# Kernel optimization log

Hardware: AMD Instinct MI355X
Metric: run time of the kernel (lower is better)

Reference implementation:

```python
import jax, jax.numpy as jnp
import numpy as np
import math

GRID = 32          # config.grid_size
DIM = 256          # sparse_head_dim = n_embd * mlp_internal_dim_multiplier // n_head
B, H = 8, 8        # batch, n_head
N = GRID * GRID    # tokens = grid_size^2


def get_freqs_2d(h, w, dim, theta=10000.0):
    """2D RoPE angles; returns (cos, sin) each of shape (h*w, dim//2)."""
    dim_half = dim // 2
    inv = 1.0 / theta ** (np.arange(0, dim_half, 2).astype(np.float32) / dim_half)
    fx = np.outer(np.arange(w, dtype=np.float32), inv)   # (w, dim_half//2)
    fy = np.outer(np.arange(h, dtype=np.float32), inv)   # (h, dim_half//2)
    fx_grid = np.broadcast_to(fx[None, :, :], (h, w, fx.shape[1]))
    fy_grid = np.broadcast_to(fy[:, None, :], (h, w, fy.shape[1]))
    ang = np.concatenate([fx_grid, fy_grid], axis=-1).reshape(h * w, dim_half)
    return jnp.asarray(np.cos(ang)), jnp.asarray(np.sin(ang))


def apply_rotary(x, cos, sin):
    # x: (B,H,N,D) viewed as complex pairs along last dim; complex multiply by e^{i*ang}
    xr = x.reshape(*x.shape[:-1], -1, 2)
    x0, x1 = xr[..., 0], xr[..., 1]          # (B,H,N,D/2)
    out_re = x0 * cos - x1 * sin
    out_im = x0 * sin + x1 * cos
    return jnp.stack([out_re, out_im], axis=-1).reshape(x.shape)


def setup_inputs() -> dict:
    key = jax.random.key(0)
    k1, k2, k3 = jax.random.split(key, 3)
    shape = (B, H, N, DIM)
    return {
        "Q": jax.random.normal(k1, shape, dtype=jnp.float32),
        "K": jax.random.normal(k2, shape, dtype=jnp.float32),
        "V": jax.random.normal(k3, shape, dtype=jnp.float32),
    }


def reference(Q, K, V):
    cos, sin = get_freqs_2d(GRID, GRID, DIM)  # (N, DIM/2) each, broadcast over B,H
    QR = apply_rotary(Q, cos, sin)
    KR = apply_rotary(K, cos, sin)
    scores = jnp.einsum('bhnd,bhmd->bhnm', QR, KR) / math.sqrt(QR.shape[-1])
    attn = jax.nn.softmax(scores, axis=-1)
    return jnp.einsum('bhnm,bhmd->bhnd', attn, V)
```

## Files before the change

### kernel.cpp

```cpp
#include <hip/hip_runtime.h>
#include <hip/hip_bf16.h>
#include <cstdint>

#define BH     64
#define NTOK   1024
#define DDIM   256
#define QT     128
#define KTILE  32
#define NITER  (NTOK / KTILE)
#define PP     40

typedef __bf16 bf16x8 __attribute__((ext_vector_type(8)));
typedef float  f32x4  __attribute__((ext_vector_type(4)));
typedef float  f32x16 __attribute__((ext_vector_type(16)));

__device__ __forceinline__ unsigned short f2bf(float f) {
    __bf16 b = (__bf16)f;
    return __builtin_bit_cast(unsigned short, b);
}
__device__ __forceinline__ float bf2f(unsigned short u) {
    return __builtin_bit_cast(float, ((unsigned int)u) << 16);
}
__device__ __forceinline__ unsigned int pack2(float lo, float hi) {
    return (unsigned int)f2bf(lo) | ((unsigned int)f2bf(hi) << 16);
}

typedef const __attribute__((address_space(1))) unsigned int* gas_t;
typedef __attribute__((address_space(3))) unsigned int* las_t;
__device__ __forceinline__ void gload16(const void* g, void* l) {
    __builtin_amdgcn_global_load_lds((gas_t)g, (las_t)l, 16, 0, 0);
}

#define ANG_C    (13.287712379549449f / 64.0f)
#define SM_SCALE (1.4426950408889634f / 16.0f)

__global__ __launch_bounds__(256) void prep(const float* __restrict__ K,
                                            const float* __restrict__ V,
                                            unsigned short* __restrict__ KR,
                                            unsigned short* __restrict__ VT) {
    __shared__ unsigned short tile[64 * 264];
    int tid = threadIdx.x;
    if (blockIdx.x < 8192) {
        int gid = blockIdx.x * 256 + tid;
        int chunk = gid & 31;
        int t = (gid >> 5) & (NTOK - 1);
        float x = (float)(t & 31), y = (float)(t >> 5);
        const float4 a = *(const float4*)(K + (size_t)gid * 8);
        const float4 b = *(const float4*)(K + (size_t)gid * 8 + 4);
        float f[8] = {a.x, a.y, a.z, a.w, b.x, b.y, b.z, b.w};
        unsigned int o[4];
#pragma unroll
        for (int p = 0; p < 4; ++p) {
            int j = chunk * 4 + p;
            float pos = (j < 64) ? x : y;
            float inv = __builtin_exp2f(-(float)(j & 63) * ANG_C);
            float s, c;
            __sincosf(pos * inv, &s, &c);
            float x0 = f[2 * p], x1 = f[2 * p + 1];
            o[p] = pack2(x0 * c - x1 * s, x0 * s + x1 * c);
        }
        uint4 ov; ov.x = o[0]; ov.y = o[1]; ov.z = o[2]; ov.w = o[3];
        *(uint4*)(KR + (size_t)gid * 8) = ov;
        return;
    }
    int vb = blockIdx.x - 8192;
    int bh = vb >> 4;
    int tbase = (vb & 15) * 64;
    const float* src = V + ((size_t)bh * NTOK + tbase) * DDIM;
#pragma unroll
    for (int i = 0; i < 8; ++i) {
        int flat = i * 2048 + tid * 8;
        int tl = flat >> 8, col = flat & 255;
        const float4 a = *(const float4*)(src + (size_t)tl * DDIM + col);
        const float4 b = *(const float4*)(src + (size_t)tl * DDIM + col + 4);
        uint4 ov;
        ov.x = pack2(a.x, a.y); ov.y = pack2(a.z, a.w);
        ov.z = pack2(b.x, b.y); ov.w = pack2(b.z, b.w);
        *(uint4*)(tile + tl * 264 + col) = ov;
    }
    __syncthreads();
    unsigned short* dst = VT + (size_t)bh * ((size_t)DDIM * NTOK) + tbase;
#pragma unroll
    for (int i = 0; i < 8; ++i) {
        int task = i * 256 + tid;
        int d = task >> 3, tq = task & 7;
        unsigned int o[4];
#pragma unroll
        for (int k = 0; k < 4; ++k) {
            unsigned short lo = tile[(tq * 8 + 2 * k    ) * 264 + d];
            unsigned short hi = tile[(tq * 8 + 2 * k + 1) * 264 + d];
            o[k] = (unsigned int)lo | ((unsigned int)hi << 16);
        }
        uint4 ov; ov.x = o[0]; ov.y = o[1]; ov.z = o[2]; ov.w = o[3];
        *(uint4*)(dst + (size_t)d * NTOK + tq * 8) = ov;
    }
}

__global__ __launch_bounds__(256, 2) void flash_attn(
        const float* __restrict__ Q,
        const unsigned short* __restrict__ KR,
        const unsigned short* __restrict__ VTg,
        float* __restrict__ Out) {
    __shared__ unsigned short KT[2][KTILE * DDIM];
    __shared__ unsigned short VTl[2][DDIM * KTILE];
    __shared__ unsigned short PB[4][32 * PP];

    const int tid = threadIdx.x;
    const int wave = tid >> 6, lane = tid & 63;
    const int l31 = lane & 31, h = lane >> 5;
    const int b = blockIdx.x;
    const int bh = (b & 7) + ((b >> 6) << 3);
    const int qbase = ((b >> 3) & 7) * QT;

    const unsigned short* krB = KR + (size_t)bh * ((size_t)NTOK * DDIM);
    const unsigned short* vtB = VTg + (size_t)bh * ((size_t)DDIM * NTOK);

    bf16x8 qfrag[16];
    {
        const int qtok = qbase + wave * 32 + l31;
        const float x = (float)(qtok & 31), y = (float)(qtok >> 5);
        const float* qrow = Q + ((size_t)bh * NTOK + qtok) * DDIM;
#pragma unroll
        for (int cc = 0; cc < 16; ++cc) {
            const float4 a = *(const float4*)(qrow + cc * 16 + h * 8);
            const float4 b2 = *(const float4*)(qrow + cc * 16 + h * 8 + 4);
            float f[8] = {a.x, a.y, a.z, a.w, b2.x, b2.y, b2.z, b2.w};
            unsigned int po[4];
#pragma unroll
            for (int p = 0; p < 4; ++p) {
                int j = cc * 8 + h * 4 + p;
                float pos = (j < 64) ? x : y;
                float inv = __builtin_exp2f(-(float)(j & 63) * ANG_C);
                float s, c;
                __sincosf(pos * inv, &s, &c);
                float x0 = f[2 * p], x1 = f[2 * p + 1];
                po[p] = pack2(x0 * c - x1 * s, x0 * s + x1 * c);
            }
            uint4 pk; pk.x = po[0]; pk.y = po[1]; pk.z = po[2]; pk.w = po[3];
            qfrag[cc] = __builtin_bit_cast(bf16x8, pk);
        }
    }
    asm volatile("s_waitcnt vmcnt(0)" ::: "memory");

    f32x16 o[8] = {};
    float lsum[16] = {};

    int kOff[4], vOff[4];
#pragma unroll
    for (int j = 0; j < 4; ++j) {
        int f = wave * 256 + j * 64 + lane;
        int rf = f >> 5, sf = f & 31;
        kOff[j] = rf * 256 + ((sf ^ (rf & 7)) * 8);
        int d0 = ((f >> 2) ^ (f >> 4)) & 1;
        int dv = ((f >> 3) << 1) | d0;
        int cv = (f & 3) ^ (dv & 3);
        vOff[j] = dv * NTOK + cv * 8;
    }
    const int kx = l31 & 7;
    const int vrd0 = ((4 * l31 + 0 + h) ^ kx) * 8;
    const int vrd1 = ((4 * l31 + 2 + h) ^ kx) * 8;

#pragma unroll
    for (int j = 0; j < 4; ++j)
        gload16(krB + kOff[j], &KT[0][wave * 2048 + j * 512]);
#pragma unroll
    for (int j = 0; j < 4; ++j)
        gload16(vtB + vOff[j], &VTl[0][wave * 2048 + j * 512]);

    unsigned short* pbw = &PB[wave][0];

    for (int it = 0; it < NITER; ++it) {
        const int cur = it & 1;
        if (it + 1 < NITER) {
            const int kb = (it + 1) * KTILE;
            const unsigned short* krT = krB + (size_t)kb * DDIM;
            const unsigned short* vtT = vtB + kb;
            const int nxt = cur ^ 1;
#pragma unroll
            for (int j = 0; j < 4; ++j)
                gload16(krT + kOff[j], &KT[nxt][wave * 2048 + j * 512]);
#pragma unroll
            for (int j = 0; j < 4; ++j)
                gload16(vtT + vOff[j], &VTl[nxt][wave * 2048 + j * 512]);
            asm volatile("s_waitcnt vmcnt(8)" ::: "memory");
        } else {
            asm volatile("s_waitcnt vmcnt(0)" ::: "memory");
        }
        __builtin_amdgcn_s_barrier();

        f32x16 sc = {};
        const unsigned short* ktb = KT[cur];
        __builtin_amdgcn_s_setprio(1);
#pragma unroll
        for (int cc = 0; cc < 16; ++cc) {
            const int sl = ((2 * cc + h) ^ kx) * 8;
            bf16x8 kb_ = *(const bf16x8*)(ktb + l31 * 256 + sl);
            sc = __builtin_amdgcn_mfma_f32_32x32x16_bf16(qfrag[cc], kb_, sc, 0, 0, 0);
        }
        __builtin_amdgcn_s_setprio(0);

#pragma unroll
        for (int r = 0; r < 16; ++r) {
            float p = __builtin_exp2f(sc[r] * SM_SCALE);
            unsigned short pb = f2bf(p);
            pbw[((r & 3) + 8 * (r >> 2) + 4 * h) * PP + l31] = pb;
            lsum[r] += bf2f(pb);
        }
        bf16x8 pa0 = *(const bf16x8*)(pbw + l31 * PP + h * 8);
        bf16x8 pa1 = *(const bf16x8*)(pbw + l31 * PP + 16 + h * 8);

        const unsigned short* vtb = VTl[cur];
        __builtin_amdgcn_s_setprio(1);
#pragma unroll
        for (int nt = 0; nt < 8; ++nt) {
            bf16x8 v0 = *(const bf16x8*)(vtb + nt * 1024 + vrd0);
            bf16x8 v1 = *(const bf16x8*)(vtb + nt * 1024 + vrd1);
            o[nt] = __builtin_amdgcn_mfma_f32_32x32x16_bf16(pa0, v0, o[nt], 0, 0, 0);
            o[nt] = __builtin_amdgcn_mfma_f32_32x32x16_bf16(pa1, v1, o[nt], 0, 0, 0);
        }
        __builtin_amdgcn_s_setprio(0);

        asm volatile("s_waitcnt lgkmcnt(0)" ::: "memory");
        __builtin_amdgcn_s_barrier();
    }

#pragma unroll
    for (int r = 0; r < 16; ++r) {
        float s = lsum[r];
        s += __shfl_xor(s, 1);
        s += __shfl_xor(s, 2);
        s += __shfl_xor(s, 4);
        s += __shfl_xor(s, 8);
        s += __shfl_xor(s, 16);
        float rl = 1.0f / s;
        const int row = (r & 3) + 8 * (r >> 2) + 4 * h;
        float* orow =
            Out + ((size_t)bh * NTOK + qbase + wave * 32 + row) * DDIM;
#pragma unroll
        for (int nt = 0; nt < 8; ++nt)
            orow[nt * 32 + l31] = o[nt][r] * rl;
    }
}

extern "C" void kernel_launch(void* const* d_in, const int* in_sizes, int n_in,
                              void* d_out, int out_size, void* d_ws, size_t ws_size,
                              hipStream_t stream) {
    const float* Q = (const float*)d_in[0];
    const float* K = (const float*)d_in[1];
    const float* V = (const float*)d_in[2];
    unsigned short* KR = (unsigned short*)d_ws;
    unsigned short* VT = KR + (size_t)BH * NTOK * DDIM;
    float* O = (float*)d_out;

    prep<<<8192 + BH * (NTOK / 64), 256, 0, stream>>>(K, V, KR, VT);
    flash_attn<<<BH * (NTOK / QT), 256, 0, stream>>>(Q, KR, VT, O);
}
```

Before: 349.0 us.

## Compute transposed scores to keep P in registers, dropping the LDS round-trip

Swaps the MFMA operands so the score tile comes out transposed (keys by queries). Each lane can then build the P operand for the PV matmul from its own registers plus cross-half shuffles, with no write to and read from an LDS scratch buffer. Row sums become per-lane partial sums reduced once at the end. The V shared-memory swizzle is redesigned to match, and RoPE sin/cos now uses the hardware revolution-based sin/cos instructions. The shuffle packing adds cross-lane traffic, and the V swizzle change could introduce bank conflicts.

```diff
diff --git a/kernel.cpp b/kernel.cpp
--- a/kernel.cpp
+++ b/kernel.cpp
@@ -8,10 +8,8 @@
 #define QT     128
 #define KTILE  32
 #define NITER  (NTOK / KTILE)
-#define PP     40
 
 typedef __bf16 bf16x8 __attribute__((ext_vector_type(8)));
-typedef float  f32x4  __attribute__((ext_vector_type(4)));
 typedef float  f32x16 __attribute__((ext_vector_type(16)));
 
 __device__ __forceinline__ unsigned short f2bf(float f) {
@@ -23,6 +21,12 @@
 }
 __device__ __forceinline__ unsigned int pack2(float lo, float hi) {
     return (unsigned int)f2bf(lo) | ((unsigned int)f2bf(hi) << 16);
+}
+
+__device__ __forceinline__ void sincos_rev(float rev, float* s, float* c) {
+    float fr = rev - __builtin_floorf(rev);
+    *s = __builtin_amdgcn_sinf(fr);
+    *c = __builtin_amdgcn_cosf(fr);
 }
 
 typedef const __attribute__((address_space(1))) unsigned int* gas_t;
@@ -32,6 +36,7 @@
 }
 
 #define ANG_C    (13.287712379549449f / 64.0f)
+#define L2_2PI   2.6514961294723187f
 #define SM_SCALE (1.4426950408889634f / 16.0f)
 
 __global__ __launch_bounds__(256) void prep(const float* __restrict__ K,
@@ -53,9 +58,9 @@
         for (int p = 0; p < 4; ++p) {
             int j = chunk * 4 + p;
             float pos = (j < 64) ? x : y;
-            float inv = __builtin_exp2f(-(float)(j & 63) * ANG_C);
+            float invr = __builtin_exp2f(-(float)(j & 63) * ANG_C - L2_2PI);
             float s, c;
-            __sincosf(pos * inv, &s, &c);
+            sincos_rev(pos * invr, &s, &c);
             float x0 = f[2 * p], x1 = f[2 * p + 1];
             o[p] = pack2(x0 * c - x1 * s, x0 * s + x1 * c);
         }
@@ -103,7 +108,6 @@
         float* __restrict__ Out) {
     __shared__ unsigned short KT[2][KTILE * DDIM];
     __shared__ unsigned short VTl[2][DDIM * KTILE];
-    __shared__ unsigned short PB[4][32 * PP];
 
     const int tid = threadIdx.x;
     const int wave = tid >> 6, lane = tid & 63;
@@ -130,9 +134,9 @@
             for (int p = 0; p < 4; ++p) {
                 int j = cc * 8 + h * 4 + p;
                 float pos = (j < 64) ? x : y;
-                float inv = __builtin_exp2f(-(float)(j & 63) * ANG_C);
+                float invr = __builtin_exp2f(-(float)(j & 63) * ANG_C - L2_2PI);
                 float s, c;
-                __sincosf(pos * inv, &s, &c);
+                sincos_rev(pos * invr, &s, &c);
                 float x0 = f[2 * p], x1 = f[2 * p + 1];
                 po[p] = pack2(x0 * c - x1 * s, x0 * s + x1 * c);
             }
@@ -143,7 +147,7 @@
     asm volatile("s_waitcnt vmcnt(0)" ::: "memory");
 
     f32x16 o[8] = {};
-    float lsum[16] = {};
+    float lsum[4] = {};
 
     int kOff[4], vOff[4];
 #pragma unroll
@@ -151,14 +155,14 @@
         int f = wave * 256 + j * 64 + lane;
         int rf = f >> 5, sf = f & 31;
         kOff[j] = rf * 256 + ((sf ^ (rf & 7)) * 8);
-        int d0 = ((f >> 2) ^ (f >> 4)) & 1;
-        int dv = ((f >> 3) << 1) | d0;
-        int cv = (f & 3) ^ (dv & 3);
-        vOff[j] = dv * NTOK + cv * 8;
+        int gI = f ^ ((f >> 3) & 3);
+        vOff[j] = (gI >> 2) * NTOK + (gI & 3) * 8;
     }
     const int kx = l31 & 7;
-    const int vrd0 = ((4 * l31 + 0 + h) ^ kx) * 8;
-    const int vrd1 = ((4 * l31 + 2 + h) ^ kx) * 8;
+    const int vx = (l31 >> 1) & 3;
+    const int vbase = l31 * 32;
+    const int vh0 = (h ^ vx) * 8;
+    const int vh1 = ((2 + h) ^ vx) * 8;
 
 #pragma unroll
     for (int j = 0; j < 4; ++j)
@@ -166,8 +170,6 @@
 #pragma unroll
     for (int j = 0; j < 4; ++j)
         gload16(vtB + vOff[j], &VTl[0][wave * 2048 + j * 512]);
-
-    unsigned short* pbw = &PB[wave][0];
 
     for (int it = 0; it < NITER; ++it) {
         const int cur = it & 1;
@@ -195,28 +197,45 @@
         for (int cc = 0; cc < 16; ++cc) {
             const int sl = ((2 * cc + h) ^ kx) * 8;
             bf16x8 kb_ = *(const bf16x8*)(ktb + l31 * 256 + sl);
-            sc = __builtin_amdgcn_mfma_f32_32x32x16_bf16(qfrag[cc], kb_, sc, 0, 0, 0);
+            sc = __builtin_amdgcn_mfma_f32_32x32x16_bf16(kb_, qfrag[cc], sc, 0, 0, 0);
         }
         __builtin_amdgcn_s_setprio(0);
 
+        unsigned short bs[16];
 #pragma unroll
         for (int r = 0; r < 16; ++r) {
             float p = __builtin_exp2f(sc[r] * SM_SCALE);
-            unsigned short pb = f2bf(p);
-            pbw[((r & 3) + 8 * (r >> 2) + 4 * h) * PP + l31] = pb;
-            lsum[r] += bf2f(pb);
-        }
-        bf16x8 pa0 = *(const bf16x8*)(pbw + l31 * PP + h * 8);
-        bf16x8 pa1 = *(const bf16x8*)(pbw + l31 * PP + 16 + h * 8);
+            bs[r] = f2bf(p);
+            lsum[r & 3] += bf2f(bs[r]);
+        }
+        bf16x8 pa[2];
+#pragma unroll
+        for (int c = 0; c < 2; ++c) {
+            unsigned int P1 = (unsigned)bs[c*8+0] | ((unsigned)bs[c*8+1] << 16);
+            unsigned int P2 = (unsigned)bs[c*8+2] | ((unsigned)bs[c*8+3] << 16);
+            unsigned int P3 = (unsigned)bs[c*8+4] | ((unsigned)bs[c*8+5] << 16);
+            unsigned int P4 = (unsigned)bs[c*8+6] | ((unsigned)bs[c*8+7] << 16);
+            unsigned int P1x = __shfl_xor((int)P1, 32);
+            unsigned int P2x = __shfl_xor((int)P2, 32);
+            unsigned int P3x = __shfl_xor((int)P3, 32);
+            unsigned int P4x = __shfl_xor((int)P4, 32);
+            uint4 w;
+            w.x = h ? P3x : P1;
+            w.y = h ? P4x : P2;
+            w.z = h ? P3  : P1x;
+            w.w = h ? P4  : P2x;
+            pa[c] = __builtin_bit_cast(bf16x8, w);
+        }
 
         const unsigned short* vtb = VTl[cur];
         __builtin_amdgcn_s_setprio(1);
 #pragma unroll
         for (int nt = 0; nt < 8; ++nt) {
-            bf16x8 v0 = *(const bf16x8*)(vtb + nt * 1024 + vrd0);
-            bf16x8 v1 = *(const bf16x8*)(vtb + nt * 1024 + vrd1);
-            o[nt] = __builtin_amdgcn_mfma_f32_32x32x16_bf16(pa0, v0, o[nt], 0, 0, 0);
-            o[nt] = __builtin_amdgcn_mfma_f32_32x32x16_bf16(pa1, v1, o[nt], 0, 0, 0);
+            const unsigned short* vp = vtb + nt * 1024 + vbase;
+            bf16x8 v0 = *(const bf16x8*)(vp + vh0);
+            bf16x8 v1 = *(const bf16x8*)(vp + vh1);
+            o[nt] = __builtin_amdgcn_mfma_f32_32x32x16_bf16(pa[0], v0, o[nt], 0, 0, 0);
+            o[nt] = __builtin_amdgcn_mfma_f32_32x32x16_bf16(pa[1], v1, o[nt], 0, 0, 0);
         }
         __builtin_amdgcn_s_setprio(0);
 
@@ -224,18 +243,14 @@
         __builtin_amdgcn_s_barrier();
     }
 
+    float tot = (lsum[0] + lsum[1]) + (lsum[2] + lsum[3]);
+    tot += __shfl_xor(tot, 32);
 #pragma unroll
     for (int r = 0; r < 16; ++r) {
-        float s = lsum[r];
-        s += __shfl_xor(s, 1);
-        s += __shfl_xor(s, 2);
-        s += __shfl_xor(s, 4);
-        s += __shfl_xor(s, 8);
-        s += __shfl_xor(s, 16);
-        float rl = 1.0f / s;
-        const int row = (r & 3) + 8 * (r >> 2) + 4 * h;
+        const int q = (r & 3) + 8 * (r >> 2) + 4 * h;
+        float rl = 1.0f / __shfl(tot, q);
         float* orow =
-            Out + ((size_t)bh * NTOK + qbase + wave * 32 + row) * DDIM;
+            Out + ((size_t)bh * NTOK + qbase + wave * 32 + q) * DDIM;
 #pragma unroll
         for (int nt = 0; nt < 8; ++nt)
             orow[nt * 32 + l31] = o[nt][r] * rl;
```

New measurement: 309.0 us. 11.5% less time.
